# Kernel optimization log

Hardware: AMD Instinct MI355X
Metric: run time of the kernel (lower is better)

## Reference

```python
import jax, jax.numpy as jnp
import numpy as np

B, C, H, W, N, NH, DFF = 2, 256, 128, 128, 8, 8, 1024
EPS = 1e-5


def _ln(x, g, b):
    m = jnp.mean(x, -1, keepdims=True)
    v = jnp.mean((x - m) ** 2, -1, keepdims=True)
    return (x - m) / jnp.sqrt(v + EPS) * g + b


def _mha(q, k, v, Wqkv, bqkv, Wo, bo, nh):
    # q,k,v: [Bq, S, C]; torch MultiheadAttention with packed in_proj
    Bq, S, Cd = q.shape
    dh = Cd // nh
    Wq, Wk, Wv = jnp.split(Wqkv, 3, axis=0)
    bq, bk, bv = jnp.split(bqkv, 3, axis=0)
    qp = (q @ Wq.T + bq).reshape(Bq, S, nh, dh).transpose(0, 2, 1, 3)
    kp = (k @ Wk.T + bk).reshape(Bq, S, nh, dh).transpose(0, 2, 1, 3)
    vp = (v @ Wv.T + bv).reshape(Bq, S, nh, dh).transpose(0, 2, 1, 3)
    scores = jnp.einsum('bhqd,bhkd->bhqk', qp, kp) / jnp.sqrt(jnp.asarray(dh, qp.dtype))
    attn = jax.nn.softmax(scores, axis=-1)
    o = jnp.einsum('bhqk,bhkd->bhqd', attn, vp).transpose(0, 2, 1, 3).reshape(Bq, S, Cd)
    return o @ Wo.T + bo


def _enc_layer(q, k, v, Wqkv, bqkv, Wo, bo, W1, b1, W2, b2, g1, be1, g2, be2, nh):
    # normalize_before=False, dropout=0
    src = _ln(v + _mha(q, k, v, Wqkv, bqkv, Wo, bo, nh), g1, be1)
    ffn = jax.nn.relu(src @ W1.T + b1) @ W2.T + b2
    return _ln(src + ffn, g2, be2)


def _encode(feat, pe, layer_params, nh):
    # feat: [Nv, hw, C]; pe = glob_pos + rel_pos broadcast: [Nv, hw, C]
    out = feat
    qk = out + pe
    out = _enc_layer(qk, qk, out, *layer_params, nh)
    out_t = out.transpose(1, 0, 2)                 # [hw, Nv, C] axis-permuted pass
    qk = out_t + pe.transpose(1, 0, 2)
    out = _enc_layer(qk, qk, out_t, *layer_params, nh).transpose(1, 0, 2)
    return out


def _forward(backbone_memory, defe_feature_filtered, glob_pos_embed,
             Wqkv, bqkv, Wo, bo, W1, b1, W2, b2, g1, be1, g2, be2,
             relW1, relb1, relW2, relb2, n):
    Bm, Cd, Hf, Wf = backbone_memory.shape
    h, w = Hf // n, Wf // n
    Nv, hw = n * n, h * w

    # relative position embedding: MLP over normalized grid coords [h,w,2]
    gy, gx = jnp.meshgrid(jnp.arange(h, dtype=jnp.float32),
                          jnp.arange(w, dtype=jnp.float32), indexing='ij')
    coords = jnp.stack([gx / (w - 1), gy / (h - 1)], axis=-1)
    rel = (jax.nn.relu(coords @ relW1.T + relb1) @ relW2.T + relb2)  # [h,w,C]
    rel = rel.reshape(1, hw, Cd)                                      # [1,hw,C]

    # window partition: [B, Nv, hw, C]
    win = backbone_memory.reshape(Bm, Cd, n, h, n, w).transpose(0, 2, 4, 1, 3, 5)
    win = win.reshape(Bm, Nv, Cd, hw).transpose(0, 1, 3, 2)

    # per-window global pos embed: [Nv, hw, C]
    glob = glob_pos_embed.reshape(Cd, n, h, n, w).transpose(1, 3, 0, 2, 4)
    glob = glob.reshape(Nv, Cd, hw).transpose(0, 2, 1)

    pe = glob + rel
    layer_params = (Wqkv, bqkv, Wo, bo, W1, b1, W2, b2, g1, be1, g2, be2)
    enc = jax.vmap(lambda f: _encode(f, pe, layer_params, NH))(win)   # [B,Nv,hw,C]

    # scatter windows back and add residually (reconstructed += feats)
    back = enc.transpose(0, 1, 3, 2).reshape(Bm, n, n, Cd, h, w)
    back = back.transpose(0, 3, 1, 4, 2, 5).reshape(Bm, Cd, Hf, Wf)
    reconstructed = backbone_memory + back

    # defe_mask via non-overlapping max-pool (all-ones mask -> all valid)
    Hm, Wm = defe_feature_filtered.shape[-2:]
    kh = (Hm // Hf) * h
    kw = (Wm // Wf) * w
    pooled = defe_feature_filtered.reshape(Bm, 1, n, kh, n, kw).max(axis=(3, 5))
    defe_mask = pooled[:, 0] > 0
    return reconstructed, defe_mask


def setup_inputs() -> dict:
    key = jax.random.key(0)
    ks = jax.random.split(key, 10)
    s = 0.02
    return {
        'backbone_memory': jax.random.normal(ks[0], (B, C, H, W), jnp.float32),
        'defe_feature_filtered': jnp.ones((B, 1, H, W), jnp.float32),
        'glob_pos_embed': jax.random.normal(ks[1], (C, H, W), jnp.float32),
        'Wqkv': jax.random.normal(ks[2], (3 * C, C), jnp.float32) * s,
        'bqkv': jnp.zeros((3 * C,), jnp.float32),
        'Wo': jax.random.normal(ks[3], (C, C), jnp.float32) * s,
        'bo': jnp.zeros((C,), jnp.float32),
        'W1': jax.random.normal(ks[4], (DFF, C), jnp.float32) * s,
        'b1': jnp.zeros((DFF,), jnp.float32),
        'W2': jax.random.normal(ks[5], (C, DFF), jnp.float32) * s,
        'b2': jnp.zeros((C,), jnp.float32),
        'g1': jnp.ones((C,), jnp.float32),
        'be1': jnp.zeros((C,), jnp.float32),
        'g2': jnp.ones((C,), jnp.float32),
        'be2': jnp.zeros((C,), jnp.float32),
        'relW1': jax.random.normal(ks[6], (64, 2), jnp.float32) * s,
        'relb1': jnp.zeros((64,), jnp.float32),
        'relW2': jax.random.normal(ks[7], (C, 64), jnp.float32) * s,
        'relb2': jnp.zeros((C,), jnp.float32),
        'n': N,
    }


def reference(backbone_memory, defe_feature_filtered, glob_pos_embed,
              Wqkv, bqkv, Wo, bo, W1, b1, W2, b2, g1, be1, g2, be2,
              relW1, relb1, relW2, relb2, n):
    return _forward(backbone_memory, defe_feature_filtered, glob_pos_embed,
                    Wqkv, bqkv, Wo, bo, W1, b1, W2, b2, g1, be1, g2, be2,
                    relW1, relb1, relW2, relb2, n)
```

## Files before the change

kernel.cpp:

```cpp
#include <hip/hip_runtime.h>
#include <hip/hip_bf16.h>

#define C_DIM 256
#define NHEAD 8
#define DH 32
#define NTOK 32768
#define PETOK 16384
#define DFF_DIM 1024
#define LN_EPS 1e-5f

typedef unsigned int u32;
typedef unsigned short ushortT;
using frag_ab = __attribute__((ext_vector_type(8))) short;
using f32x4   = __attribute__((ext_vector_type(4))) float;

__device__ __forceinline__ float bflo(u32 u) { union { u32 i; float f; } c; c.i = u << 16; return c.f; }
__device__ __forceinline__ float bfhi(u32 u) { union { u32 i; float f; } c; c.i = u & 0xffff0000u; return c.f; }
__device__ __forceinline__ float b2f(ushortT u) { union { u32 i; float f; } c; c.i = ((u32)u) << 16; return c.f; }
__device__ __forceinline__ ushortT f2b(float f) {
    __hip_bfloat16 b = __float2bfloat16(f);
    return *reinterpret_cast<ushortT*>(&b);
}
__device__ __forceinline__ u32 packbf(float lo, float hi) {
    return (u32)f2b(lo) | ((u32)f2b(hi) << 16);
}
__device__ __forceinline__ void gload_lds16(const ushortT* g, ushortT* l) {
    __builtin_amdgcn_global_load_lds((const __attribute__((address_space(1))) void*)g,
                                     (__attribute__((address_space(3))) void*)l, 16, 0, 0);
}

__global__ void cvt_all_kernel(const float* __restrict__ Wqkv, const float* __restrict__ Wo,
                               const float* __restrict__ W1, const float* __restrict__ W2,
                               ushortT* __restrict__ dst) {
    const int i = (blockIdx.x * 256 + threadIdx.x) * 4;
    const float* src;
    int off;
    if (i < 196608)      { src = Wqkv; off = 0; }
    else if (i < 262144) { src = Wo;   off = 196608; }
    else if (i < 524288) { src = W1;   off = 262144; }
    else                 { src = W2;   off = 524288; }
    const float4 v = *(const float4*)&src[i - off];
    uint2 o = {packbf(v.x, v.y), packbf(v.z, v.w)};
    *(uint2*)&dst[i] = o;
}

__global__ void rel_kernel(const float* __restrict__ relW1, const float* __restrict__ relb1,
                           const float* __restrict__ relW2, const float* __restrict__ relb2,
                           float* __restrict__ rel) {
    __shared__ float hid[64];
    int t = blockIdx.x;
    int ty = t >> 4, tx = t & 15;
    float cx = tx * (1.0f / 15.0f);
    float cy = ty * (1.0f / 15.0f);
    int c = threadIdx.x;
    if (c < 64) {
        float h = relW1[c * 2 + 0] * cx + relW1[c * 2 + 1] * cy + relb1[c];
        hid[c] = fmaxf(h, 0.0f);
    }
    __syncthreads();
    float acc = relb2[c];
    #pragma unroll
    for (int jj = 0; jj < 64; ++jj) acc = fmaf(hid[jj], relW2[c * 64 + jj], acc);
    rel[t * C_DIM + c] = acc;
}

__global__ __launch_bounds__(256) void pe_kernel(const float* __restrict__ glob,
                                                 const float* __restrict__ rel,
                                                 ushortT* __restrict__ peb) {
    __shared__ float tile[32][129];
    const int y = blockIdx.x;
    const int c0 = blockIdx.y * 32;
    const int i = y >> 4, ty = y & 15;
    const int tid = threadIdx.x;
    const int xl = tid & 127;
    #pragma unroll
    for (int p = 0; p < 16; ++p) {
        const int cl = p * 2 + (tid >> 7);
        tile[cl][xl] = glob[(size_t)(c0 + cl) * 16384 + y * 128 + xl];
    }
    __syncthreads();
    const int cl = tid & 31;
    #pragma unroll
    for (int p = 0; p < 16; ++p) {
        const int x = p * 8 + (tid >> 5);
        const int v = i * 8 + (x >> 4);
        const int t = ty * 16 + (x & 15);
        const float val = tile[cl][x] + rel[t * C_DIM + c0 + cl];
        peb[(size_t)(v * 256 + t) * C_DIM + c0 + cl] = f2b(val);
    }
}

__global__ __launch_bounds__(256) void window_kernel(const float* __restrict__ backbone,
                                                     ushortT* __restrict__ Xb) {
    __shared__ float tile[32][129];
    const int y = blockIdx.x;
    const int c0 = blockIdx.y * 32;
    const int b = blockIdx.z;
    const int i = y >> 4, ty = y & 15;
    const int tid = threadIdx.x;
    const int xl = tid & 127;
    #pragma unroll
    for (int p = 0; p < 16; ++p) {
        const int cl = p * 2 + (tid >> 7);
        tile[cl][xl] = backbone[(size_t)b * 4194304 + (size_t)(c0 + cl) * 16384 + y * 128 + xl];
    }
    __syncthreads();
    const int cl = tid & 31;
    #pragma unroll
    for (int p = 0; p < 16; ++p) {
        const int x = p * 8 + (tid >> 5);
        const int v = i * 8 + (x >> 4);
        const int t = ty * 16 + (x & 15);
        const size_t tok = (size_t)b * PETOK + v * 256 + t;
        Xb[tok * C_DIM + c0 + cl] = f2b(tile[cl][x]);
    }
}

__global__ __launch_bounds__(256) void scatter_kernel(const float* __restrict__ backbone,
                                                      const ushortT* __restrict__ X,
                                                      float* __restrict__ out) {
    __shared__ ushortT tile[128][34];
    const int y = blockIdx.x;
    const int c0 = blockIdx.y * 32;
    const int b = blockIdx.z;
    const int i = y >> 4, ty = y & 15;
    const int tid = threadIdx.x;
    const int cl = tid & 31;
    #pragma unroll
    for (int p = 0; p < 16; ++p) {
        const int x = p * 8 + (tid >> 5);
        const int v = i * 8 + (x >> 4);
        const int t = ty * 16 + (x & 15);
        const size_t tok = (size_t)b * PETOK + v * 256 + t;
        tile[x][cl] = X[tok * C_DIM + c0 + cl];
    }
    __syncthreads();
    const int xl = tid & 127;
    #pragma unroll
    for (int p = 0; p < 16; ++p) {
        const int c = c0 + p * 2 + (tid >> 7);
        const size_t gi = (size_t)b * 4194304 + (size_t)c * 16384 + y * 128 + xl;
        out[gi] = backbone[gi] + b2f(tile[xl][p * 2 + (tid >> 7)]);
    }
}

#define BM 128
#define BN 128
#define BK 32

template<bool FUSE_PE, bool RELU>
__global__ __launch_bounds__(256) void gemm_bf16(
        const ushortT* __restrict__ A, int lda,
        const ushortT* __restrict__ peb,
        const ushortT* __restrict__ W,
        const float* __restrict__ bias,
        ushortT* __restrict__ Cout, int ldc, int K) {
    __shared__ ushortT As[BM][BK];
    __shared__ ushortT Bs[BN][BK];
    const int nwg = gridDim.x * gridDim.y;
    const int flat = blockIdx.y * gridDim.x + blockIdx.x;
    const int cpx = nwg >> 3;
    const int swz = (flat & 7) * cpx + (flat >> 3);
    const int m0 = (swz / gridDim.x) * BM;
    const int n0 = (swz % gridDim.x) * BN;
    const int tid = threadIdx.x;
    const int lane = tid & 63;
    const int wave = tid >> 6;
    const int wm = (wave >> 1) * 64;
    const int wn = (wave & 1) * 64;
    const int fr = lane & 15;
    const int fg = lane >> 4;
    const int gRow = wave * 32 + (lane >> 2);
    const int gCol = (lane & 3) * 8;
    const int sRow = tid >> 2;
    const int sCol = (tid & 3) * 8;

    f32x4 acc[4][4];
    #pragma unroll
    for (int i = 0; i < 4; ++i)
        #pragma unroll
        for (int j = 0; j < 4; ++j)
            acc[i][j] = (f32x4){0.f, 0.f, 0.f, 0.f};

    for (int k0 = 0; k0 < K; k0 += BK) {
        if (FUSE_PE) {
            #pragma unroll
            for (int h = 0; h < 2; ++h) {
                const int row = sRow + h * 64;
                uint4 av = *(const uint4*)&A[(size_t)(m0 + row) * lda + k0 + sCol];
                const uint4 pv = *(const uint4*)&peb[(size_t)((m0 + row) & 16383) * C_DIM + k0 + sCol];
                u32* a = (u32*)&av;
                const u32* p = (const u32*)&pv;
                #pragma unroll
                for (int e = 0; e < 4; ++e)
                    a[e] = packbf(bflo(a[e]) + bflo(p[e]), bfhi(a[e]) + bfhi(p[e]));
                *(uint4*)&As[row][sCol] = av;
            }
        } else {
            gload_lds16(&A[(size_t)(m0 + gRow) * lda + k0 + gCol], &As[wave * 32][0]);
            gload_lds16(&A[(size_t)(m0 + gRow + 16) * lda + k0 + gCol], &As[wave * 32 + 16][0]);
        }
        gload_lds16(&W[(size_t)(n0 + gRow) * K + k0 + gCol], &Bs[wave * 32][0]);
        gload_lds16(&W[(size_t)(n0 + gRow + 16) * K + k0 + gCol], &Bs[wave * 32 + 16][0]);
        __syncthreads();
        frag_ab af[4], bf[4];
        #pragma unroll
        for (int i = 0; i < 4; ++i) af[i] = *(const frag_ab*)&As[wm + i * 16 + fr][fg * 8];
        #pragma unroll
        for (int j = 0; j < 4; ++j) bf[j] = *(const frag_ab*)&Bs[wn + j * 16 + fr][fg * 8];
        #pragma unroll
        for (int i = 0; i < 4; ++i)
            #pragma unroll
            for (int j = 0; j < 4; ++j)
                acc[i][j] = __builtin_amdgcn_mfma_f32_16x16x32_bf16(af[i], bf[j], acc[i][j], 0, 0, 0);
        __syncthreads();
    }
    #pragma unroll
    for (int j = 0; j < 4; ++j) {
        const float bv = bias[n0 + wn + j * 16 + fr];
        #pragma unroll
        for (int i = 0; i < 4; ++i) {
            #pragma unroll
            for (int r = 0; r < 4; ++r) {
                float v = acc[i][j][r] + bv;
                if (RELU) v = fmaxf(v, 0.0f);
                const int m = m0 + wm + i * 16 + fg * 4 + r;
                const int n = n0 + wn + j * 16 + fr;
                Cout[(size_t)m * ldc + n] = f2b(v);
            }
        }
    }
}

#define KVC 128
__global__ __launch_bounds__(256) void attn_p0(const ushortT* __restrict__ QKb,
                                               const ushortT* __restrict__ Vb,
                                               ushortT* __restrict__ Ob) {
    __shared__ ushortT K_lds[KVC * 40];
    __shared__ ushortT V_t[32 * 136];
    __shared__ ushortT P_lds[4][16 * 136];
    const int grp = blockIdx.x;
    const int h = grp & 7;
    const int bv = grp >> 3;
    const int base = (bv >> 6) * PETOK + (bv & 63) * 256;
    const int tid = threadIdx.x;
    const int wave = tid >> 6;
    const int lane = tid & 63;
    const int fr = lane & 15;
    const int fg = lane >> 4;
    const float scale = 0.17677669529663687f;

    frag_ab qf[4];
    size_t qtok[4];
    #pragma unroll
    for (int s = 0; s < 4; ++s) {
        qtok[s] = (size_t)(base + wave * 64 + s * 16 + fr);
        qf[s] = *(const frag_ab*)&QKb[qtok[s] * 512 + h * DH + fg * 8];
    }
    float m[4], l[4];
    f32x4 o0[4], o1[4];
    #pragma unroll
    for (int s = 0; s < 4; ++s) {
        m[s] = -1e30f; l[s] = 0.f;
        o0[s] = (f32x4){0.f, 0.f, 0.f, 0.f};
        o1[s] = (f32x4){0.f, 0.f, 0.f, 0.f};
    }

    for (int c = 0; c < 2; ++c) {
        __syncthreads();
        #pragma unroll
        for (int it = 0; it < 2; ++it) {
            const int idx = it * 256 + tid;
            const int row = idx >> 2, ch = idx & 3;
            const size_t tok = (size_t)(base + c * KVC + row);
            const uint4 kv = *(const uint4*)&QKb[tok * 512 + 256 + h * DH + ch * 8];
            *(uint4*)&K_lds[row * 40 + ch * 8] = kv;
            const uint4 vv = *(const uint4*)&Vb[tok * C_DIM + h * DH + ch * 8];
            const ushortT* vp = (const ushortT*)&vv;
            #pragma unroll
            for (int e = 0; e < 8; ++e) V_t[(ch * 8 + e) * 136 + row] = vp[e];
        }
        __syncthreads();
        #pragma unroll
        for (int s = 0; s < 4; ++s) {
            f32x4 sc[8];
            #pragma unroll
            for (int kt = 0; kt < 8; ++kt) {
                const frag_ab kf = *(const frag_ab*)&K_lds[(kt * 16 + fr) * 40 + fg * 8];
                sc[kt] = __builtin_amdgcn_mfma_f32_16x16x32_bf16(kf, qf[s], (f32x4){0.f, 0.f, 0.f, 0.f}, 0, 0, 0);
            }
            float mx = -1e30f;
            #pragma unroll
            for (int kt = 0; kt < 8; ++kt)
                mx = fmaxf(mx, fmaxf(fmaxf(sc[kt][0], sc[kt][1]), fmaxf(sc[kt][2], sc[kt][3])));
            mx = fmaxf(mx, __shfl_xor(mx, 16, 64));
            mx = fmaxf(mx, __shfl_xor(mx, 32, 64));
            const float nm = fmaxf(m[s], mx);
            const float corr = __expf((m[s] - nm) * scale);
            m[s] = nm;
            float lsum = 0.f;
            #pragma unroll
            for (int kt = 0; kt < 8; ++kt) {
                const float p0 = __expf((sc[kt][0] - nm) * scale);
                const float p1 = __expf((sc[kt][1] - nm) * scale);
                const float p2 = __expf((sc[kt][2] - nm) * scale);
                const float p3 = __expf((sc[kt][3] - nm) * scale);
                lsum += (p0 + p1) + (p2 + p3);
                uint2 pk;
                pk.x = packbf(p0, p1);
                pk.y = packbf(p2, p3);
                *(uint2*)&P_lds[wave][fr * 136 + kt * 16 + fg * 4] = pk;
            }
            lsum += __shfl_xor(lsum, 16, 64);
            lsum += __shfl_xor(lsum, 32, 64);
            l[s] = l[s] * corr + lsum;
            o0[s] *= corr;
            o1[s] *= corr;
            #pragma unroll
            for (int kc = 0; kc < 4; ++kc) {
                const frag_ab pf = *(const frag_ab*)&P_lds[wave][fr * 136 + kc * 32 + fg * 8];
                const frag_ab v0 = *(const frag_ab*)&V_t[fr * 136 + kc * 32 + fg * 8];
                const frag_ab v1 = *(const frag_ab*)&V_t[(16 + fr) * 136 + kc * 32 + fg * 8];
                o0[s] = __builtin_amdgcn_mfma_f32_16x16x32_bf16(v0, pf, o0[s], 0, 0, 0);
                o1[s] = __builtin_amdgcn_mfma_f32_16x16x32_bf16(v1, pf, o1[s], 0, 0, 0);
            }
        }
    }
    #pragma unroll
    for (int s = 0; s < 4; ++s) {
        const float inv = 1.0f / l[s];
        ushortT* ob = &Ob[qtok[s] * C_DIM + h * DH];
        uint2 w0, w1;
        w0.x = packbf(o0[s][0] * inv, o0[s][1] * inv);
        w0.y = packbf(o0[s][2] * inv, o0[s][3] * inv);
        w1.x = packbf(o1[s][0] * inv, o1[s][1] * inv);
        w1.y = packbf(o1[s][2] * inv, o1[s][3] * inv);
        *(uint2*)&ob[fg * 4] = w0;
        *(uint2*)&ob[16 + fg * 4] = w1;
    }
}

__global__ __launch_bounds__(256) void attn_p1(const ushortT* __restrict__ QKb,
                                               const ushortT* __restrict__ Vb,
                                               ushortT* __restrict__ Ob) {
    __shared__ ushortT K_lds[4][64 * 40];
    __shared__ ushortT V_t[4][32 * 72];
    __shared__ ushortT P_lds[4][16 * 72];
    const int wave = threadIdx.x >> 6;
    const int lane = threadIdx.x & 63;
    const int unit = blockIdx.x * 4 + wave;
    const int h = unit & 7;
    const int g = unit >> 3;
    const int base = (g >> 8) * PETOK + (g & 255);
    const int fr = lane & 15;
    const int fg = lane >> 4;
    const float scale = 0.17677669529663687f;
    #pragma unroll
    for (int it = 0; it < 4; ++it) {
        const int idx = it * 64 + lane;
        const int row = idx >> 2, ch = idx & 3;
        const size_t tok = (size_t)(base + row * 256);
        const uint4 kv = *(const uint4*)&QKb[tok * 512 + 256 + h * DH + ch * 8];
        *(uint4*)&K_lds[wave][row * 40 + ch * 8] = kv;
        const uint4 vv = *(const uint4*)&Vb[tok * C_DIM + h * DH + ch * 8];
        const ushortT* vp = (const ushortT*)&vv;
        #pragma unroll
        for (int e = 0; e < 8; ++e) V_t[wave][(ch * 8 + e) * 72 + row] = vp[e];
    }
    #pragma unroll
    for (int s = 0; s < 4; ++s) {
        const int qq = s * 16 + fr;
        const size_t qtok = (size_t)(base + qq * 256);
        const frag_ab qf = *(const frag_ab*)&QKb[qtok * 512 + h * DH + fg * 8];
        f32x4 sc[4];
        #pragma unroll
        for (int kt = 0; kt < 4; ++kt) {
            const frag_ab kf = *(const frag_ab*)&K_lds[wave][(kt * 16 + fr) * 40 + fg * 8];
            sc[kt] = __builtin_amdgcn_mfma_f32_16x16x32_bf16(kf, qf, (f32x4){0.f, 0.f, 0.f, 0.f}, 0, 0, 0);
        }
        float mx = -1e30f;
        #pragma unroll
        for (int kt = 0; kt < 4; ++kt)
            mx = fmaxf(mx, fmaxf(fmaxf(sc[kt][0], sc[kt][1]), fmaxf(sc[kt][2], sc[kt][3])));
        mx = fmaxf(mx, __shfl_xor(mx, 16, 64));
        mx = fmaxf(mx, __shfl_xor(mx, 32, 64));
        float lsum = 0.f;
        #pragma unroll
        for (int kt = 0; kt < 4; ++kt) {
            const float p0 = __expf((sc[kt][0] - mx) * scale);
            const float p1 = __expf((sc[kt][1] - mx) * scale);
            const float p2 = __expf((sc[kt][2] - mx) * scale);
            const float p3 = __expf((sc[kt][3] - mx) * scale);
            lsum += (p0 + p1) + (p2 + p3);
            uint2 pk;
            pk.x = packbf(p0, p1);
            pk.y = packbf(p2, p3);
            *(uint2*)&P_lds[wave][fr * 72 + kt * 16 + fg * 4] = pk;
        }
        lsum += __shfl_xor(lsum, 16, 64);
        lsum += __shfl_xor(lsum, 32, 64);
        f32x4 o0 = {0.f, 0.f, 0.f, 0.f}, o1 = {0.f, 0.f, 0.f, 0.f};
        #pragma unroll
        for (int kc = 0; kc < 2; ++kc) {
            const frag_ab pf = *(const frag_ab*)&P_lds[wave][fr * 72 + kc * 32 + fg * 8];
            const frag_ab v0 = *(const frag_ab*)&V_t[wave][fr * 72 + kc * 32 + fg * 8];
            const frag_ab v1 = *(const frag_ab*)&V_t[wave][(16 + fr) * 72 + kc * 32 + fg * 8];
            o0 = __builtin_amdgcn_mfma_f32_16x16x32_bf16(v0, pf, o0, 0, 0, 0);
            o1 = __builtin_amdgcn_mfma_f32_16x16x32_bf16(v1, pf, o1, 0, 0, 0);
        }
        const float inv = 1.0f / lsum;
        ushortT* ob = &Ob[qtok * C_DIM + h * DH];
        uint2 w0, w1;
        w0.x = packbf(o0[0] * inv, o0[1] * inv);
        w0.y = packbf(o0[2] * inv, o0[3] * inv);
        w1.x = packbf(o1[0] * inv, o1[1] * inv);
        w1.y = packbf(o1[2] * inv, o1[3] * inv);
        *(uint2*)&ob[fg * 4] = w0;
        *(uint2*)&ob[16 + fg * 4] = w1;
    }
}

__global__ __launch_bounds__(256) void ln_kernel(ushortT* __restrict__ X, const ushortT* __restrict__ Y,
                                                 const float* __restrict__ g, const float* __restrict__ be) {
    int tok = blockIdx.x * 4 + (threadIdx.x >> 6);
    int lane = threadIdx.x & 63;
    const uint2 xu = *(const uint2*)&X[(size_t)tok * C_DIM + lane * 4];
    const uint2 yu = *(const uint2*)&Y[(size_t)tok * C_DIM + lane * 4];
    float v0 = bflo(xu.x) + bflo(yu.x), v1 = bfhi(xu.x) + bfhi(yu.x);
    float v2 = bflo(xu.y) + bflo(yu.y), v3 = bfhi(xu.y) + bfhi(yu.y);
    float s = v0 + v1 + v2 + v3;
    float ss = v0 * v0 + v1 * v1 + v2 * v2 + v3 * v3;
    #pragma unroll
    for (int off = 32; off; off >>= 1) {
        s += __shfl_xor(s, off, 64);
        ss += __shfl_xor(ss, off, 64);
    }
    float mean = s * (1.0f / 256.0f);
    float var = ss * (1.0f / 256.0f) - mean * mean;
    float inv = rsqrtf(var + LN_EPS);
    const float4 gv = *(const float4*)&g[lane * 4];
    const float4 bv = *(const float4*)&be[lane * 4];
    float o0 = (v0 - mean) * inv * gv.x + bv.x;
    float o1 = (v1 - mean) * inv * gv.y + bv.y;
    float o2 = (v2 - mean) * inv * gv.z + bv.z;
    float o3 = (v3 - mean) * inv * gv.w + bv.w;
    uint2 ob = {packbf(o0, o1), packbf(o2, o3)};
    *(uint2*)&X[(size_t)tok * C_DIM + lane * 4] = ob;
}

__global__ void mask_kernel(const float* __restrict__ defe, float* __restrict__ out) {
    __shared__ float wmax[4];
    const int idx = blockIdx.x;
    const int b = idx >> 6;
    const int ii = (idx >> 3) & 7;
    const int jj = idx & 7;
    const int t = threadIdx.x;
    const int y = t >> 4, xx = t & 15;
    float v = defe[b * 16384 + (ii * 16 + y) * 128 + jj * 16 + xx];
    #pragma unroll
    for (int off = 32; off; off >>= 1) v = fmaxf(v, __shfl_xor(v, off, 64));
    if ((t & 63) == 0) wmax[t >> 6] = v;
    __syncthreads();
    if (t == 0) {
        float mx = fmaxf(fmaxf(wmax[0], wmax[1]), fmaxf(wmax[2], wmax[3]));
        out[8388608 + idx] = (mx > 0.0f) ? 1.0f : 0.0f;
    }
}

extern "C" void kernel_launch(void* const* d_in, const int* in_sizes, int n_in,
                              void* d_out, int out_size, void* d_ws, size_t ws_size,
                              hipStream_t stream) {
    const float* backbone = (const float*)d_in[0];
    const float* defe     = (const float*)d_in[1];
    const float* glob     = (const float*)d_in[2];
    const float* Wqkv     = (const float*)d_in[3];
    const float* bqkv     = (const float*)d_in[4];
    const float* Wo       = (const float*)d_in[5];
    const float* bo       = (const float*)d_in[6];
    const float* W1       = (const float*)d_in[7];
    const float* b1       = (const float*)d_in[8];
    const float* W2       = (const float*)d_in[9];
    const float* b2       = (const float*)d_in[10];
    const float* g1       = (const float*)d_in[11];
    const float* be1      = (const float*)d_in[12];
    const float* g2       = (const float*)d_in[13];
    const float* be2      = (const float*)d_in[14];
    const float* relW1    = (const float*)d_in[15];
    const float* relb1    = (const float*)d_in[16];
    const float* relW2    = (const float*)d_in[17];
    const float* relb2    = (const float*)d_in[18];

    ushortT* peb    = (ushortT*)d_ws;
    ushortT* Wqkv_b = peb + 4194304;
    ushortT* Wo_b   = Wqkv_b + 196608;
    ushortT* W1_b   = Wo_b + 65536;
    ushortT* W2_b   = W1_b + 262144;
    ushortT* Xb     = W2_b + 262144;
    ushortT* QKb    = Xb + 8388608;
    ushortT* Vb     = QKb + 16777216;
    ushortT* Ob     = Vb + 8388608;
    ushortT* Hb     = QKb;
    ushortT* Yb     = Ob + 8388608;
    float*   relf   = (float*)(Yb + 8388608);
    size_t needed = (size_t)((char*)(relf + 65536) - (char*)d_ws);
    if (ws_size < needed) return;

    cvt_all_kernel<<<768, 256, 0, stream>>>(Wqkv, Wo, W1, W2, Wqkv_b);
    rel_kernel<<<256, 256, 0, stream>>>(relW1, relb1, relW2, relb2, relf);
    pe_kernel<<<dim3(128, 8), 256, 0, stream>>>(glob, relf, peb);
    window_kernel<<<dim3(128, 8, 2), 256, 0, stream>>>(backbone, Xb);

    for (int pass = 0; pass < 2; ++pass) {
        gemm_bf16<true, false><<<dim3(512 / BN, NTOK / BM), 256, 0, stream>>>(
            Xb, C_DIM, peb, Wqkv_b, bqkv, QKb, 512, C_DIM);
        gemm_bf16<false, false><<<dim3(256 / BN, NTOK / BM), 256, 0, stream>>>(
            Xb, C_DIM, nullptr, Wqkv_b + 512 * 256, bqkv + 512, Vb, C_DIM, C_DIM);
        if (pass == 0) {
            attn_p0<<<128 * NHEAD, 256, 0, stream>>>(QKb, Vb, Ob);
        } else {
            attn_p1<<<4096 / 4, 256, 0, stream>>>(QKb, Vb, Ob);
        }
        gemm_bf16<false, false><<<dim3(256 / BN, NTOK / BM), 256, 0, stream>>>(
            Ob, C_DIM, nullptr, Wo_b, bo, Yb, C_DIM, C_DIM);
        ln_kernel<<<NTOK / 4, 256, 0, stream>>>(Xb, Yb, g1, be1);
        gemm_bf16<false, true><<<dim3(DFF_DIM / BN, NTOK / BM), 256, 0, stream>>>(
            Xb, C_DIM, nullptr, W1_b, b1, Hb, DFF_DIM, C_DIM);
        gemm_bf16<false, false><<<dim3(256 / BN, NTOK / BM), 256, 0, stream>>>(
            Hb, DFF_DIM, nullptr, W2_b, b2, Yb, C_DIM, DFF_DIM);
        ln_kernel<<<NTOK / 4, 256, 0, stream>>>(Xb, Yb, g2, be2);
    }

    scatter_kernel<<<dim3(128, 8, 2), 256, 0, stream>>>(backbone, Xb, (float*)d_out);
    mask_kernel<<<128, 256, 0, stream>>>(defe, (float*)d_out);
}
```

Baseline: 352.5 us.

## Fuse output projection and FFN2 GEMMs with residual LayerNorm epilogue

Adds a gemm_ln kernel in which each block computes a full 64x256 output row tile, stages the bias-added result in LDS, then applies the residual add and LayerNorm in place on X. This replaces the separate GEMM-then-ln_kernel pairs after attention and after the FFN, removing the Y intermediate buffer and its write and read round-trip plus four launches. The trade-off is a new tiling with only 512 blocks of 512 threads and no double buffering in the K loop, which may lower GEMM efficiency, especially for K=1024.

```diff
diff --git a/kernel.cpp b/kernel.cpp
--- a/kernel.cpp
+++ b/kernel.cpp
@@ -232,6 +232,115 @@
     }
 }
 
+__global__ __launch_bounds__(512) void gemm_ln(
+        const ushortT* __restrict__ A,
+        const ushortT* __restrict__ W,
+        const float* __restrict__ bias,
+        const float* __restrict__ g, const float* __restrict__ be,
+        ushortT* __restrict__ Xr, int K) {
+    __shared__ ushortT smem[64 * 264];
+    ushortT* As = smem;
+    ushortT* Bs = smem + 2048;
+    const int m0 = blockIdx.x * 64;
+    const int tid = threadIdx.x;
+    const int lane = tid & 63;
+    const int wave = tid >> 6;
+    const int wm = (wave >> 2) * 32;
+    const int wn = (wave & 3) * 64;
+    const int fr = lane & 15;
+    const int fg = lane >> 4;
+    const int gR = lane >> 2;
+    const int gC = (lane & 3) * 8;
+
+    f32x4 acc[2][4];
+    #pragma unroll
+    for (int i = 0; i < 2; ++i)
+        #pragma unroll
+        for (int j = 0; j < 4; ++j)
+            acc[i][j] = (f32x4){0.f, 0.f, 0.f, 0.f};
+
+    for (int k0 = 0; k0 < K; k0 += BK) {
+        if (wave < 4)
+            gload_lds16(&A[(size_t)(m0 + wave * 16 + gR) * K + k0 + gC], &As[wave * 16 * 32]);
+        gload_lds16(&W[(size_t)(wave * 32 + gR) * K + k0 + gC], &Bs[wave * 32 * 32]);
+        gload_lds16(&W[(size_t)(wave * 32 + 16 + gR) * K + k0 + gC], &Bs[(wave * 32 + 16) * 32]);
+        __syncthreads();
+        frag_ab af[2], bf[4];
+        #pragma unroll
+        for (int i = 0; i < 2; ++i) af[i] = *(const frag_ab*)&As[(wm + i * 16 + fr) * 32 + fg * 8];
+        #pragma unroll
+        for (int j = 0; j < 4; ++j) bf[j] = *(const frag_ab*)&Bs[(wn + j * 16 + fr) * 32 + fg * 8];
+        #pragma unroll
+        for (int i = 0; i < 2; ++i)
+            #pragma unroll
+            for (int j = 0; j < 4; ++j)
+                acc[i][j] = __builtin_amdgcn_mfma_f32_16x16x32_bf16(af[i], bf[j], acc[i][j], 0, 0, 0);
+        __syncthreads();
+    }
+    ushortT* Yl = smem;
+    #pragma unroll
+    for (int j = 0; j < 4; ++j) {
+        const int n = wn + j * 16 + fr;
+        const float bv = bias[n];
+        #pragma unroll
+        for (int i = 0; i < 2; ++i)
+            #pragma unroll
+            for (int r = 0; r < 4; ++r)
+                Yl[(wm + i * 16 + fg * 4 + r) * 264 + n] = f2b(acc[i][j][r] + bv);
+    }
+    __syncthreads();
+    const int row = tid >> 3;
+    const int part = tid & 7;
+    const size_t tok = (size_t)(m0 + row);
+    float vv[4][8];
+    float s = 0.f, ss = 0.f;
+    #pragma unroll
+    for (int q = 0; q < 4; ++q) {
+        const uint4 yu = *(const uint4*)&Yl[row * 264 + part * 32 + q * 8];
+        const uint4 xu = *(const uint4*)&Xr[tok * C_DIM + part * 32 + q * 8];
+        const u32 yw[4] = {yu.x, yu.y, yu.z, yu.w};
+        const u32 xw[4] = {xu.x, xu.y, xu.z, xu.w};
+        #pragma unroll
+        for (int e = 0; e < 4; ++e) {
+            const float a = bflo(yw[e]) + bflo(xw[e]);
+            const float b = bfhi(yw[e]) + bfhi(xw[e]);
+            vv[q][2 * e] = a;
+            vv[q][2 * e + 1] = b;
+            s += a + b;
+            ss += a * a + b * b;
+        }
+    }
+    #pragma unroll
+    for (int off = 1; off <= 4; off <<= 1) {
+        s += __shfl_xor(s, off, 64);
+        ss += __shfl_xor(ss, off, 64);
+    }
+    const float mean = s * (1.0f / 256.0f);
+    const float var = ss * (1.0f / 256.0f) - mean * mean;
+    const float inv = rsqrtf(var + LN_EPS);
+    #pragma unroll
+    for (int q = 0; q < 4; ++q) {
+        const float4 ga = *(const float4*)&g[part * 32 + q * 8];
+        const float4 gb = *(const float4*)&g[part * 32 + q * 8 + 4];
+        const float4 ba = *(const float4*)&be[part * 32 + q * 8];
+        const float4 bb = *(const float4*)&be[part * 32 + q * 8 + 4];
+        const float o0 = (vv[q][0] - mean) * inv * ga.x + ba.x;
+        const float o1 = (vv[q][1] - mean) * inv * ga.y + ba.y;
+        const float o2 = (vv[q][2] - mean) * inv * ga.z + ba.z;
+        const float o3 = (vv[q][3] - mean) * inv * ga.w + ba.w;
+        const float o4 = (vv[q][4] - mean) * inv * gb.x + bb.x;
+        const float o5 = (vv[q][5] - mean) * inv * gb.y + bb.y;
+        const float o6 = (vv[q][6] - mean) * inv * gb.z + bb.z;
+        const float o7 = (vv[q][7] - mean) * inv * gb.w + bb.w;
+        uint4 ou;
+        ou.x = packbf(o0, o1);
+        ou.y = packbf(o2, o3);
+        ou.z = packbf(o4, o5);
+        ou.w = packbf(o6, o7);
+        *(uint4*)&Xr[tok * C_DIM + part * 32 + q * 8] = ou;
+    }
+}
+
 #define KVC 128
 __global__ __launch_bounds__(256) void attn_p0(const ushortT* __restrict__ QKb,
                                                const ushortT* __restrict__ Vb,
@@ -418,34 +527,6 @@
         *(uint2*)&ob[fg * 4] = w0;
         *(uint2*)&ob[16 + fg * 4] = w1;
     }
-}
-
-__global__ __launch_bounds__(256) void ln_kernel(ushortT* __restrict__ X, const ushortT* __restrict__ Y,
-                                                 const float* __restrict__ g, const float* __restrict__ be) {
-    int tok = blockIdx.x * 4 + (threadIdx.x >> 6);
-    int lane = threadIdx.x & 63;
-    const uint2 xu = *(const uint2*)&X[(size_t)tok * C_DIM + lane * 4];
-    const uint2 yu = *(const uint2*)&Y[(size_t)tok * C_DIM + lane * 4];
-    float v0 = bflo(xu.x) + bflo(yu.x), v1 = bfhi(xu.x) + bfhi(yu.x);
-    float v2 = bflo(xu.y) + bflo(yu.y), v3 = bfhi(xu.y) + bfhi(yu.y);
-    float s = v0 + v1 + v2 + v3;
-    float ss = v0 * v0 + v1 * v1 + v2 * v2 + v3 * v3;
-    #pragma unroll
-    for (int off = 32; off; off >>= 1) {
-        s += __shfl_xor(s, off, 64);
-        ss += __shfl_xor(ss, off, 64);
-    }
-    float mean = s * (1.0f / 256.0f);
-    float var = ss * (1.0f / 256.0f) - mean * mean;
-    float inv = rsqrtf(var + LN_EPS);
-    const float4 gv = *(const float4*)&g[lane * 4];
-    const float4 bv = *(const float4*)&be[lane * 4];
-    float o0 = (v0 - mean) * inv * gv.x + bv.x;
-    float o1 = (v1 - mean) * inv * gv.y + bv.y;
-    float o2 = (v2 - mean) * inv * gv.z + bv.z;
-    float o3 = (v3 - mean) * inv * gv.w + bv.w;
-    uint2 ob = {packbf(o0, o1), packbf(o2, o3)};
-    *(uint2*)&X[(size_t)tok * C_DIM + lane * 4] = ob;
 }
 
 __global__ void mask_kernel(const float* __restrict__ defe, float* __restrict__ out) {
@@ -500,8 +581,7 @@
     ushortT* Vb     = QKb + 16777216;
     ushortT* Ob     = Vb + 8388608;
     ushortT* Hb     = QKb;
-    ushortT* Yb     = Ob + 8388608;
-    float*   relf   = (float*)(Yb + 8388608);
+    float*   relf   = (float*)(Ob + 8388608);
     size_t needed = (size_t)((char*)(relf + 65536) - (char*)d_ws);
     if (ws_size < needed) return;
 
@@ -520,14 +600,10 @@
         } else {
             attn_p1<<<4096 / 4, 256, 0, stream>>>(QKb, Vb, Ob);
         }
-        gemm_bf16<false, false><<<dim3(256 / BN, NTOK / BM), 256, 0, stream>>>(
-            Ob, C_DIM, nullptr, Wo_b, bo, Yb, C_DIM, C_DIM);
-        ln_kernel<<<NTOK / 4, 256, 0, stream>>>(Xb, Yb, g1, be1);
+        gemm_ln<<<NTOK / 64, 512, 0, stream>>>(Ob, Wo_b, bo, g1, be1, Xb, C_DIM);
         gemm_bf16<false, true><<<dim3(DFF_DIM / BN, NTOK / BM), 256, 0, stream>>>(
             Xb, C_DIM, nullptr, W1_b, b1, Hb, DFF_DIM, C_DIM);
-        gemm_bf16<false, false><<<dim3(256 / BN, NTOK / BM), 256, 0, stream>>>(
-            Hb, DFF_DIM, nullptr, W2_b, b2, Yb, C_DIM, DFF_DIM);
-        ln_kernel<<<NTOK / 4, 256, 0, stream>>>(Xb, Yb, g2, be2);
+        gemm_ln<<<NTOK / 64, 512, 0, stream>>>(Hb, W2_b, b2, g2, be2, Xb, DFF_DIM);
     }
 
     scatter_kernel<<<dim3(128, 8, 2), 256, 0, stream>>>(backbone, Xb, (float*)d_out);
```

Result: no change. 354.8 us (+0.6%).

## Merge QK and V projections into one GEMM and precompute X+PE upstream

Applied to the files above, without the earlier changes.

The QK and V projection GEMMs become one 768-wide GEMM writing an interleaved QKV buffer. Tiles with column offset 512 or more read plain X, and the others read a precomputed X+PE buffer. That buffer is produced by the window kernel and by the second LayerNorm of pass 0, so the GEMM no longer adds PE on the fly and can use direct global-to-LDS loads. The change removes one launch and the repeated PE reads and adds done per N-tile. In exchange it costs an extra X+PE write and read and a larger QKV buffer with a 768-element stride.

```diff
diff --git a/kernel.cpp b/kernel.cpp
--- a/kernel.cpp
+++ b/kernel.cpp
@@ -91,7 +91,9 @@
 }
 
 __global__ __launch_bounds__(256) void window_kernel(const float* __restrict__ backbone,
-                                                     ushortT* __restrict__ Xb) {
+                                                     const ushortT* __restrict__ peb,
+                                                     ushortT* __restrict__ Xb,
+                                                     ushortT* __restrict__ XPEb) {
     __shared__ float tile[32][129];
     const int y = blockIdx.x;
     const int c0 = blockIdx.y * 32;
@@ -111,8 +113,11 @@
         const int x = p * 8 + (tid >> 5);
         const int v = i * 8 + (x >> 4);
         const int t = ty * 16 + (x & 15);
-        const size_t tok = (size_t)b * PETOK + v * 256 + t;
-        Xb[tok * C_DIM + c0 + cl] = f2b(tile[cl][x]);
+        const size_t vt = (size_t)(v * 256 + t);
+        const size_t tok = (size_t)b * PETOK + vt;
+        const float val = tile[cl][x];
+        Xb[tok * C_DIM + c0 + cl] = f2b(val);
+        XPEb[tok * C_DIM + c0 + cl] = f2b(val + b2f(peb[vt * C_DIM + c0 + cl]));
     }
 }
 
@@ -148,10 +153,11 @@
 #define BN 128
 #define BK 32
 
-template<bool FUSE_PE, bool RELU>
+template<bool QKVMODE, bool RELU>
 __global__ __launch_bounds__(256) void gemm_bf16(
-        const ushortT* __restrict__ A, int lda,
-        const ushortT* __restrict__ peb,
+        const ushortT* __restrict__ A,
+        const ushortT* __restrict__ A2,
+        int lda,
         const ushortT* __restrict__ W,
         const float* __restrict__ bias,
         ushortT* __restrict__ Cout, int ldc, int K) {
@@ -163,6 +169,7 @@
     const int swz = (flat & 7) * cpx + (flat >> 3);
     const int m0 = (swz / gridDim.x) * BM;
     const int n0 = (swz % gridDim.x) * BN;
+    const ushortT* Ause = (QKVMODE && n0 >= 512) ? A2 : A;
     const int tid = threadIdx.x;
     const int lane = tid & 63;
     const int wave = tid >> 6;
@@ -172,8 +179,6 @@
     const int fg = lane >> 4;
     const int gRow = wave * 32 + (lane >> 2);
     const int gCol = (lane & 3) * 8;
-    const int sRow = tid >> 2;
-    const int sCol = (tid & 3) * 8;
 
     f32x4 acc[4][4];
     #pragma unroll
@@ -183,23 +188,8 @@
             acc[i][j] = (f32x4){0.f, 0.f, 0.f, 0.f};
 
     for (int k0 = 0; k0 < K; k0 += BK) {
-        if (FUSE_PE) {
-            #pragma unroll
-            for (int h = 0; h < 2; ++h) {
-                const int row = sRow + h * 64;
-                uint4 av = *(const uint4*)&A[(size_t)(m0 + row) * lda + k0 + sCol];
-                const uint4 pv = *(const uint4*)&peb[(size_t)((m0 + row) & 16383) * C_DIM + k0 + sCol];
-                u32* a = (u32*)&av;
-                const u32* p = (const u32*)&pv;
-                #pragma unroll
-                for (int e = 0; e < 4; ++e)
-                    a[e] = packbf(bflo(a[e]) + bflo(p[e]), bfhi(a[e]) + bfhi(p[e]));
-                *(uint4*)&As[row][sCol] = av;
-            }
-        } else {
-            gload_lds16(&A[(size_t)(m0 + gRow) * lda + k0 + gCol], &As[wave * 32][0]);
-            gload_lds16(&A[(size_t)(m0 + gRow + 16) * lda + k0 + gCol], &As[wave * 32 + 16][0]);
-        }
+        gload_lds16(&Ause[(size_t)(m0 + gRow) * lda + k0 + gCol], &As[wave * 32][0]);
+        gload_lds16(&Ause[(size_t)(m0 + gRow + 16) * lda + k0 + gCol], &As[wave * 32 + 16][0]);
         gload_lds16(&W[(size_t)(n0 + gRow) * K + k0 + gCol], &Bs[wave * 32][0]);
         gload_lds16(&W[(size_t)(n0 + gRow + 16) * K + k0 + gCol], &Bs[wave * 32 + 16][0]);
         __syncthreads();
@@ -233,8 +223,7 @@
 }
 
 #define KVC 128
-__global__ __launch_bounds__(256) void attn_p0(const ushortT* __restrict__ QKb,
-                                               const ushortT* __restrict__ Vb,
+__global__ __launch_bounds__(256) void attn_p0(const ushortT* __restrict__ QKVb,
                                                ushortT* __restrict__ Ob) {
     __shared__ ushortT K_lds[KVC * 40];
     __shared__ ushortT V_t[32 * 136];
@@ -255,7 +244,7 @@
     #pragma unroll
     for (int s = 0; s < 4; ++s) {
         qtok[s] = (size_t)(base + wave * 64 + s * 16 + fr);
-        qf[s] = *(const frag_ab*)&QKb[qtok[s] * 512 + h * DH + fg * 8];
+        qf[s] = *(const frag_ab*)&QKVb[qtok[s] * 768 + h * DH + fg * 8];
     }
     float m[4], l[4];
     f32x4 o0[4], o1[4];
@@ -273,9 +262,9 @@
             const int idx = it * 256 + tid;
             const int row = idx >> 2, ch = idx & 3;
             const size_t tok = (size_t)(base + c * KVC + row);
-            const uint4 kv = *(const uint4*)&QKb[tok * 512 + 256 + h * DH + ch * 8];
+            const uint4 kv = *(const uint4*)&QKVb[tok * 768 + 256 + h * DH + ch * 8];
             *(uint4*)&K_lds[row * 40 + ch * 8] = kv;
-            const uint4 vv = *(const uint4*)&Vb[tok * C_DIM + h * DH + ch * 8];
+            const uint4 vv = *(const uint4*)&QKVb[tok * 768 + 512 + h * DH + ch * 8];
             const ushortT* vp = (const ushortT*)&vv;
             #pragma unroll
             for (int e = 0; e < 8; ++e) V_t[(ch * 8 + e) * 136 + row] = vp[e];
@@ -340,8 +329,7 @@
     }
 }
 
-__global__ __launch_bounds__(256) void attn_p1(const ushortT* __restrict__ QKb,
-                                               const ushortT* __restrict__ Vb,
+__global__ __launch_bounds__(256) void attn_p1(const ushortT* __restrict__ QKVb,
                                                ushortT* __restrict__ Ob) {
     __shared__ ushortT K_lds[4][64 * 40];
     __shared__ ushortT V_t[4][32 * 72];
@@ -360,9 +348,9 @@
         const int idx = it * 64 + lane;
         const int row = idx >> 2, ch = idx & 3;
         const size_t tok = (size_t)(base + row * 256);
-        const uint4 kv = *(const uint4*)&QKb[tok * 512 + 256 + h * DH + ch * 8];
+        const uint4 kv = *(const uint4*)&QKVb[tok * 768 + 256 + h * DH + ch * 8];
         *(uint4*)&K_lds[wave][row * 40 + ch * 8] = kv;
-        const uint4 vv = *(const uint4*)&Vb[tok * C_DIM + h * DH + ch * 8];
+        const uint4 vv = *(const uint4*)&QKVb[tok * 768 + 512 + h * DH + ch * 8];
         const ushortT* vp = (const ushortT*)&vv;
         #pragma unroll
         for (int e = 0; e < 8; ++e) V_t[wave][(ch * 8 + e) * 72 + row] = vp[e];
@@ -371,7 +359,7 @@
     for (int s = 0; s < 4; ++s) {
         const int qq = s * 16 + fr;
         const size_t qtok = (size_t)(base + qq * 256);
-        const frag_ab qf = *(const frag_ab*)&QKb[qtok * 512 + h * DH + fg * 8];
+        const frag_ab qf = *(const frag_ab*)&QKVb[qtok * 768 + h * DH + fg * 8];
         f32x4 sc[4];
         #pragma unroll
         for (int kt = 0; kt < 4; ++kt) {
@@ -420,8 +408,11 @@
     }
 }
 
+template<bool WXPE>
 __global__ __launch_bounds__(256) void ln_kernel(ushortT* __restrict__ X, const ushortT* __restrict__ Y,
-                                                 const float* __restrict__ g, const float* __restrict__ be) {
+                                                 const float* __restrict__ g, const float* __restrict__ be,
+                                                 const ushortT* __restrict__ peb,
+                                                 ushortT* __restrict__ XPE) {
     int tok = blockIdx.x * 4 + (threadIdx.x >> 6);
     int lane = threadIdx.x & 63;
     const uint2 xu = *(const uint2*)&X[(size_t)tok * C_DIM + lane * 4];
@@ -446,6 +437,14 @@
     float o3 = (v3 - mean) * inv * gv.w + bv.w;
     uint2 ob = {packbf(o0, o1), packbf(o2, o3)};
     *(uint2*)&X[(size_t)tok * C_DIM + lane * 4] = ob;
+    if (WXPE) {
+        const size_t vt = (size_t)(tok & 16383);
+        const uint2 pu = *(const uint2*)&peb[vt * C_DIM + lane * 4];
+        uint2 xp;
+        xp.x = packbf(o0 + bflo(pu.x), o1 + bfhi(pu.x));
+        xp.y = packbf(o2 + bflo(pu.y), o3 + bfhi(pu.y));
+        *(uint2*)&XPE[(size_t)tok * C_DIM + lane * 4] = xp;
+    }
 }
 
 __global__ void mask_kernel(const float* __restrict__ defe, float* __restrict__ out) {
@@ -496,10 +495,10 @@
     ushortT* W1_b   = Wo_b + 65536;
     ushortT* W2_b   = W1_b + 262144;
     ushortT* Xb     = W2_b + 262144;
-    ushortT* QKb    = Xb + 8388608;
-    ushortT* Vb     = QKb + 16777216;
-    ushortT* Ob     = Vb + 8388608;
-    ushortT* Hb     = QKb;
+    ushortT* XPEb   = Xb + 8388608;
+    ushortT* QKVb   = XPEb + 8388608;
+    ushortT* Ob     = QKVb + 25165824;
+    ushortT* Hb     = QKVb;
     ushortT* Yb     = Ob + 8388608;
     float*   relf   = (float*)(Yb + 8388608);
     size_t needed = (size_t)((char*)(relf + 65536) - (char*)d_ws);
@@ -508,26 +507,28 @@
     cvt_all_kernel<<<768, 256, 0, stream>>>(Wqkv, Wo, W1, W2, Wqkv_b);
     rel_kernel<<<256, 256, 0, stream>>>(relW1, relb1, relW2, relb2, relf);
     pe_kernel<<<dim3(128, 8), 256, 0, stream>>>(glob, relf, peb);
-    window_kernel<<<dim3(128, 8, 2), 256, 0, stream>>>(backbone, Xb);
+    window_kernel<<<dim3(128, 8, 2), 256, 0, stream>>>(backbone, peb, Xb, XPEb);
 
     for (int pass = 0; pass < 2; ++pass) {
-        gemm_bf16<true, false><<<dim3(512 / BN, NTOK / BM), 256, 0, stream>>>(
-            Xb, C_DIM, peb, Wqkv_b, bqkv, QKb, 512, C_DIM);
+        gemm_bf16<true, false><<<dim3(768 / BN, NTOK / BM), 256, 0, stream>>>(
+            XPEb, Xb, C_DIM, Wqkv_b, bqkv, QKVb, 768, C_DIM);
+        if (pass == 0) {
+            attn_p0<<<128 * NHEAD, 256, 0, stream>>>(QKVb, Ob);
+        } else {
+            attn_p1<<<4096 / 4, 256, 0, stream>>>(QKVb, Ob);
+        }
         gemm_bf16<false, false><<<dim3(256 / BN, NTOK / BM), 256, 0, stream>>>(
-            Xb, C_DIM, nullptr, Wqkv_b + 512 * 256, bqkv + 512, Vb, C_DIM, C_DIM);
+            Ob, nullptr, C_DIM, Wo_b, bo, Yb, C_DIM, C_DIM);
+        ln_kernel<false><<<NTOK / 4, 256, 0, stream>>>(Xb, Yb, g1, be1, nullptr, nullptr);
+        gemm_bf16<false, true><<<dim3(DFF_DIM / BN, NTOK / BM), 256, 0, stream>>>(
+            Xb, nullptr, C_DIM, W1_b, b1, Hb, DFF_DIM, C_DIM);
+        gemm_bf16<false, false><<<dim3(256 / BN, NTOK / BM), 256, 0, stream>>>(
+            Hb, nullptr, DFF_DIM, W2_b, b2, Yb, C_DIM, DFF_DIM);
         if (pass == 0) {
-            attn_p0<<<128 * NHEAD, 256, 0, stream>>>(QKb, Vb, Ob);
+            ln_kernel<true><<<NTOK / 4, 256, 0, stream>>>(Xb, Yb, g2, be2, peb, XPEb);
         } else {
-            attn_p1<<<4096 / 4, 256, 0, stream>>>(QKb, Vb, Ob);
-        }
-        gemm_bf16<false, false><<<dim3(256 / BN, NTOK / BM), 256, 0, stream>>>(
-            Ob, C_DIM, nullptr, Wo_b, bo, Yb, C_DIM, C_DIM);
-        ln_kernel<<<NTOK / 4, 256, 0, stream>>>(Xb, Yb, g1, be1);
-        gemm_bf16<false, true><<<dim3(DFF_DIM / BN, NTOK / BM), 256, 0, stream>>>(
-            Xb, C_DIM, nullptr, W1_b, b1, Hb, DFF_DIM, C_DIM);
-        gemm_bf16<false, false><<<dim3(256 / BN, NTOK / BM), 256, 0, stream>>>(
-            Hb, DFF_DIM, nullptr, W2_b, b2, Yb, C_DIM, DFF_DIM);
-        ln_kernel<<<NTOK / 4, 256, 0, stream>>>(Xb, Yb, g2, be2);
+            ln_kernel<false><<<NTOK / 4, 256, 0, stream>>>(Xb, Yb, g2, be2, nullptr, nullptr);
+        }
     }
 
     scatter_kernel<<<dim3(128, 8, 2), 256, 0, stream>>>(backbone, Xb, (float*)d_out);
```

Result: faster. 335.8 us (-4.7%).
